# Kernel optimization log

Measured on AMD Instinct MI355X. Metric: run time of the kernel, lower is better.

The kernel has to match this reference:

```python
import jax, jax.numpy as jnp
import numpy as np

OUT_FEATURES = 11008  # LLaMA-7B FFN intermediate
IN_FEATURES = 4096    # d_model
N_TOKENS = 16         # small M -> weight-traffic bound
SCALE = 0.01
ZERO_POINT = 0


def setup_inputs() -> dict:
    key = jax.random.key(0)
    k1, k2 = jax.random.split(key)
    x = jax.random.normal(k1, (N_TOKENS, IN_FEATURES), dtype=jnp.float32)
    weight_int8 = jax.random.randint(
        k2, (OUT_FEATURES, IN_FEATURES), -128, 128, dtype=jnp.int32
    ).astype(jnp.int8)
    return {
        "x": x,
        "weight_int8": weight_int8,
        "scale": SCALE,
        "zero_point": ZERO_POINT,
    }


def reference(x, weight_int8, scale, zero_point):
    # Dequantize INT8 weight to fp32 (same elementwise pass as the torch module)
    weight_fp = (weight_int8.astype(jnp.float32) - zero_point) * scale  # [out, in]
    # F.linear(x, W) == x @ W.T
    return jnp.einsum("ti,oi->to", x, weight_fp)
```

## Files before the change

### kernel.cpp

```cpp
#include <hip/hip_runtime.h>
#include <hip/hip_bf16.h>
#include <stdint.h>


#define M_TOK 16
#define K_DIM 4096
#define N_OUT 11008

typedef int v4i __attribute__((ext_vector_type(4)));

__global__ __launch_bounds__(256) void quant_x_kernel(
    const float* __restrict__ x, int8_t* __restrict__ xh,
    int8_t* __restrict__ xl, float* __restrict__ s1_out,
    float* __restrict__ sumx_out) {
  const int t = blockIdx.x;
  const int tid = threadIdx.x;
  const float4* xv = (const float4*)(x + (long)t * K_DIM) + tid * 4;

  float vals[16];
  float m = 0.0f, s = 0.0f;
#pragma unroll
  for (int j = 0; j < 4; ++j) {
    float4 f = xv[j];
    vals[j * 4 + 0] = f.x; vals[j * 4 + 1] = f.y;
    vals[j * 4 + 2] = f.z; vals[j * 4 + 3] = f.w;
    m = fmaxf(m, fmaxf(fmaxf(fabsf(f.x), fabsf(f.y)),
                       fmaxf(fabsf(f.z), fabsf(f.w))));
    s += f.x + f.y + f.z + f.w;
  }
#pragma unroll
  for (int off = 32; off > 0; off >>= 1) {
    m = fmaxf(m, __shfl_xor(m, off));
    s += __shfl_xor(s, off);
  }
  __shared__ float lm[4], ls[4];
  const int w = tid >> 6;
  if ((tid & 63) == 0) { lm[w] = m; ls[w] = s; }
  __syncthreads();
  m = fmaxf(fmaxf(lm[0], lm[1]), fmaxf(lm[2], lm[3]));
  s = ls[0] + ls[1] + ls[2] + ls[3];

  const float s1 = (m > 0.0f) ? (m * (1.0f / 127.0f)) : 1.0f;
  const float inv = 1.0f / s1;
  if (tid == 0) { s1_out[t] = s1; sumx_out[t] = s; }

  int hq[16], lq[16];
#pragma unroll
  for (int j = 0; j < 16; ++j) {
    float xf = vals[j];
    float h = rintf(xf * inv);
    h = fminf(fmaxf(h, -127.0f), 127.0f);
    float resid = xf - h * s1;
    float l = rintf(resid * inv * 256.0f);
    l = fminf(fmaxf(l, -128.0f), 127.0f);
    hq[j] = (int)h;
    lq[j] = (int)l;
  }
  int4 hv, lv;
  int* hp = (int*)&hv;
  int* lp = (int*)&lv;
#pragma unroll
  for (int d = 0; d < 4; ++d) {
    uint32_t hw = 0, lw = 0;
#pragma unroll
    for (int j = 0; j < 4; ++j) {
      hw |= (uint32_t)(hq[d * 4 + j] & 0xff) << (8 * j);
      lw |= (uint32_t)(lq[d * 4 + j] & 0xff) << (8 * j);
    }
    hp[d] = (int)hw;
    lp[d] = (int)lw;
  }
  ((int4*)xh)[(long)t * 256 + tid] = hv;
  ((int4*)xl)[(long)t * 256 + tid] = lv;
}

__global__ __launch_bounds__(256) void qgemm_kernel(
    const int* __restrict__ W, const int8_t* __restrict__ xh,
    const int8_t* __restrict__ xl, const float* __restrict__ s1,
    const float* __restrict__ sumx, const float* __restrict__ scale_p,
    const int* __restrict__ zp_p, float* __restrict__ out) {
  const int tid = threadIdx.x;
  const int lane = tid & 63;
  const int w = tid >> 6;
  const int obase = blockIdx.x * 16;
  const int n = lane & 15;
  const int g = lane >> 4;

  __shared__ uint32_t wbuf[16 * 1024];
  __shared__ float red[4][16 * 17];

  const v4i* slab = (const v4i*)(W + (long)obase * K_DIM);
#pragma unroll
  for (int b = 0; b < 16; ++b) {
    v4i q0 = slab[(b * 4 + 0) * 256 + tid];
    v4i q1 = slab[(b * 4 + 1) * 256 + tid];
    v4i q2 = slab[(b * 4 + 2) * 256 + tid];
    v4i q3 = slab[(b * 4 + 3) * 256 + tid];
#pragma unroll
    for (int u = 0; u < 4; ++u) {
      v4i q = (u == 0) ? q0 : (u == 1) ? q1 : (u == 2) ? q2 : q3;
      const int idx = (b * 4 + u) * 256 + tid;
      const int row = idx >> 10;
      const int k4 = idx & 1023;
      uint32_t p = ((uint32_t)q.x & 0xffu) |
                   (((uint32_t)q.y & 0xffu) << 8) |
                   (((uint32_t)q.z & 0xffu) << 16) |
                   (((uint32_t)q.w & 0xffu) << 24);
      const int wr = (row << 10) | (((k4 >> 2) ^ (row & 7)) << 2) | (k4 & 3);
      wbuf[wr] = p;
    }
  }
  __syncthreads();

  const v4i* Ah = (const v4i*)xh + n * 256 + w * 64 + g;
  const v4i* Al = (const v4i*)xl + n * 256 + w * 64 + g;
  v4i accH = {0, 0, 0, 0};
  v4i accL = {0, 0, 0, 0};
#pragma unroll
  for (int it = 0; it < 16; ++it) {
    const int j = w * 64 + it * 4 + g;
    const v4i b = *(const v4i*)&wbuf[(n << 10) | ((j ^ (n & 7)) << 2)];
    accH = __builtin_amdgcn_mfma_i32_16x16x64_i8(Ah[it * 4], b, accH, 0, 0, 0);
    accL = __builtin_amdgcn_mfma_i32_16x16x64_i8(Al[it * 4], b, accL, 0, 0, 0);
  }

#pragma unroll
  for (int r = 0; r < 4; ++r) {
    float f = (float)accH[r] + (float)accL[r] * (1.0f / 256.0f);
    const int t = g * 4 + r;
    red[w][t * 17 + n] = f;
  }
  __syncthreads();

  const int t = tid >> 4;
  const int col = tid & 15;
  const float sum = red[0][t * 17 + col] + red[1][t * 17 + col] +
                    red[2][t * 17 + col] + red[3][t * 17 + col];
  const float sc = scale_p[0];
  const float zp = (float)zp_p[0];
  const float o = sc * (s1[t] * sum) - sc * zp * sumx[t];
  out[(long)t * N_OUT + obase + col] = o;
}

extern "C" void kernel_launch(void* const* d_in, const int* in_sizes, int n_in,
                              void* d_out, int out_size, void* d_ws,
                              size_t ws_size, hipStream_t stream) {
  const float* x = (const float*)d_in[0];
  const int* Wq = (const int*)d_in[1];
  const float* scale_p = (const float*)d_in[2];
  const int* zp_p = (const int*)d_in[3];
  float* out = (float*)d_out;

  int8_t* xh = (int8_t*)d_ws;
  int8_t* xl = xh + (long)M_TOK * K_DIM;
  float* s1 = (float*)(xl + (long)M_TOK * K_DIM);
  float* sumx = s1 + M_TOK;

  quant_x_kernel<<<M_TOK, 256, 0, stream>>>(x, xh, xl, s1, sumx);
  qgemm_kernel<<<N_OUT / 16, 256, 0, stream>>>(Wq, xh, xl, s1, sumx, scale_p,
                                               zp_p, out);
}
```

Before: 266.9 us.

## Halve output rows per block to double grid size and cut LDS footprint

Measured after the change: 266.9 us. About the same (+0.0%).

```diff
diff --git a/kernel.cpp b/kernel.cpp
--- a/kernel.cpp
+++ b/kernel.cpp
@@ -82,33 +82,33 @@
   const int tid = threadIdx.x;
   const int lane = tid & 63;
   const int w = tid >> 6;
-  const int obase = blockIdx.x * 16;
+  const int obase = blockIdx.x * 8;
   const int n = lane & 15;
   const int g = lane >> 4;
+  const int brow = n & 7;
 
-  __shared__ uint32_t wbuf[16 * 1024];
-  __shared__ float red[4][16 * 17];
+  __shared__ uint32_t wbuf[8 * 1024];
+  __shared__ float red[4][16 * 9];
 
   const v4i* slab = (const v4i*)(W + (long)obase * K_DIM);
+#pragma unroll 1
+  for (int b = 0; b < 4; ++b) {
+    v4i q[8];
 #pragma unroll
-  for (int b = 0; b < 16; ++b) {
-    v4i q0 = slab[(b * 4 + 0) * 256 + tid];
-    v4i q1 = slab[(b * 4 + 1) * 256 + tid];
-    v4i q2 = slab[(b * 4 + 2) * 256 + tid];
-    v4i q3 = slab[(b * 4 + 3) * 256 + tid];
+    for (int i = 0; i < 8; ++i) q[i] = slab[b * 2048 + i * 256 + tid];
 #pragma unroll
-    for (int u = 0; u < 4; ++u) {
-      v4i q = (u == 0) ? q0 : (u == 1) ? q1 : (u == 2) ? q2 : q3;
-      const int idx = (b * 4 + u) * 256 + tid;
-      const int row = idx >> 10;
-      const int k4 = idx & 1023;
-      uint32_t p = ((uint32_t)q.x & 0xffu) |
-                   (((uint32_t)q.y & 0xffu) << 8) |
-                   (((uint32_t)q.z & 0xffu) << 16) |
-                   (((uint32_t)q.w & 0xffu) << 24);
-      const int wr = (row << 10) | (((k4 >> 2) ^ (row & 7)) << 2) | (k4 & 3);
+    for (int i = 0; i < 8; ++i) {
+      const int idx4 = b * 2048 + i * 256 + tid;
+      const int row = idx4 >> 10;
+      const int k4v = idx4 & 1023;
+      uint32_t p = ((uint32_t)q[i].x & 0xffu) |
+                   (((uint32_t)q[i].y & 0xffu) << 8) |
+                   (((uint32_t)q[i].z & 0xffu) << 16) |
+                   (((uint32_t)q[i].w & 0xffu) << 24);
+      const int wr = (row << 10) | (((k4v >> 2) ^ row) << 2) | (k4v & 3);
       wbuf[wr] = p;
     }
+    __builtin_amdgcn_sched_barrier(0);
   }
   __syncthreads();
 
@@ -118,28 +118,33 @@
   v4i accL = {0, 0, 0, 0};
 #pragma unroll
   for (int it = 0; it < 16; ++it) {
-    const int j = w * 64 + it * 4 + g;
-    const v4i b = *(const v4i*)&wbuf[(n << 10) | ((j ^ (n & 7)) << 2)];
-    accH = __builtin_amdgcn_mfma_i32_16x16x64_i8(Ah[it * 4], b, accH, 0, 0, 0);
-    accL = __builtin_amdgcn_mfma_i32_16x16x64_i8(Al[it * 4], b, accL, 0, 0, 0);
+    const int slot = w * 64 + it * 4 + g;
+    const v4i bfrag =
+        *(const v4i*)&wbuf[(brow << 10) | ((slot ^ brow) << 2)];
+    accH = __builtin_amdgcn_mfma_i32_16x16x64_i8(Ah[it * 4], bfrag, accH,
+                                                 0, 0, 0);
+    accL = __builtin_amdgcn_mfma_i32_16x16x64_i8(Al[it * 4], bfrag, accL,
+                                                 0, 0, 0);
   }
 
 #pragma unroll
   for (int r = 0; r < 4; ++r) {
     float f = (float)accH[r] + (float)accL[r] * (1.0f / 256.0f);
     const int t = g * 4 + r;
-    red[w][t * 17 + n] = f;
+    if (n < 8) red[w][t * 9 + n] = f;
   }
   __syncthreads();
 
-  const int t = tid >> 4;
-  const int col = tid & 15;
-  const float sum = red[0][t * 17 + col] + red[1][t * 17 + col] +
-                    red[2][t * 17 + col] + red[3][t * 17 + col];
-  const float sc = scale_p[0];
-  const float zp = (float)zp_p[0];
-  const float o = sc * (s1[t] * sum) - sc * zp * sumx[t];
-  out[(long)t * N_OUT + obase + col] = o;
+  if (tid < 128) {
+    const int t = tid >> 3;
+    const int col = tid & 7;
+    const float sum = red[0][t * 9 + col] + red[1][t * 9 + col] +
+                      red[2][t * 9 + col] + red[3][t * 9 + col];
+    const float sc = scale_p[0];
+    const float zp = (float)zp_p[0];
+    const float o = sc * (s1[t] * sum) - sc * zp * sumx[t];
+    out[(long)t * N_OUT + obase + col] = o;
+  }
 }
 
 extern "C" void kernel_launch(void* const* d_in, const int* in_sizes, int n_in,
@@ -157,6 +162,6 @@
   float* sumx = s1 + M_TOK;
 
   quant_x_kernel<<<M_TOK, 256, 0, stream>>>(x, xh, xl, s1, sumx);
-  qgemm_kernel<<<N_OUT / 16, 256, 0, stream>>>(Wq, xh, xl, s1, sumx, scale_p,
-                                               zp_p, out);
+  qgemm_kernel<<<N_OUT / 8, 256, 0, stream>>>(Wq, xh, xl, s1, sumx, scale_p,
+                                              zp_p, out);
 }
```
